# Performance work log

Hardware: AMD Instinct MI355X
Metric: run time of the kernel (lower is better)

Reference implementation:

```python
import jax, jax.numpy as jnp
import numpy as np

B, F, E, V = 16384, 32, 16, 100000
D, S, K = 4, 8, 2            # domains, shared experts, specific experts per domain
I = F * E                    # input_dim = 512
OUT = 16
EPS = 1e-5


def _bn(x):
    # torch BatchNorm1d training mode: biased variance over batch
    m = jnp.mean(x, axis=0)
    v = jnp.var(x, axis=0)
    return (x - m) / jnp.sqrt(v + EPS)


def setup_inputs() -> dict:
    key = jax.random.key(0)
    ks = jax.random.split(key, 24)
    inp = {
        "ids": jax.random.randint(ks[0], (B, F), 0, V),
        "domain_id": jax.random.randint(ks[1], (B,), 0, D),
        "emb_table": jax.random.normal(ks[2], (F, V, E), jnp.float32) * 0.05,
        "domain_weight": jax.random.normal(ks[3], (D, I), jnp.float32) * 0.06,
        "domain_bias": jax.random.uniform(ks[4], (D, I), jnp.float32),
        # shared experts: BN affine + Linear(I->16)
        "sh_gamma": jnp.ones((S, I), jnp.float32),
        "sh_beta": jnp.zeros((S, I), jnp.float32),
        "sh_W": jax.random.normal(ks[5], (S, I, OUT), jnp.float32) * 0.04,
        "sh_b": jnp.zeros((S, OUT), jnp.float32),
        # domain-specific experts
        "sp_gamma": jnp.ones((D, K, I), jnp.float32),
        "sp_beta": jnp.zeros((D, K, I), jnp.float32),
        "sp_W": jax.random.normal(ks[6], (D, K, I, OUT), jnp.float32) * 0.04,
        "sp_b": jnp.zeros((D, K, OUT), jnp.float32),
        # gate
        "gate_W": jax.random.normal(ks[7], (I, S + K), jnp.float32) * 0.04,
        "gate_b": jnp.zeros((S + K,), jnp.float32),
        # final MLP 16 -> 32 -> 32 -> 1 (Linear+BN+ReLU per hidden layer)
        "mlp_W1": jax.random.normal(ks[8], (OUT, 32), jnp.float32) * 0.25,
        "mlp_b1": jnp.zeros((32,), jnp.float32),
        "mlp_g1": jnp.ones((32,), jnp.float32),
        "mlp_be1": jnp.zeros((32,), jnp.float32),
        "mlp_W2": jax.random.normal(ks[9], (32, 32), jnp.float32) * 0.18,
        "mlp_b2": jnp.zeros((32,), jnp.float32),
        "mlp_g2": jnp.ones((32,), jnp.float32),
        "mlp_be2": jnp.zeros((32,), jnp.float32),
        "mlp_W3": jax.random.normal(ks[10], (32, 1), jnp.float32) * 0.18,
        "mlp_b3": jnp.zeros((1,), jnp.float32),
    }
    return inp


def reference(ids, domain_id, emb_table, domain_weight, domain_bias,
              sh_gamma, sh_beta, sh_W, sh_b,
              sp_gamma, sp_beta, sp_W, sp_b,
              gate_W, gate_b,
              mlp_W1, mlp_b1, mlp_g1, mlp_be1,
              mlp_W2, mlp_b2, mlp_g2, mlp_be2,
              mlp_W3, mlp_b3):
    # embedding lookup: per-field table gather -> [B, F, E] -> [B, I]
    emb = emb_table[jnp.arange(F)[None, :], ids].reshape(B, I)

    # torch.where over domain masks collapses to a gather of per-domain affine
    shared_emb = emb * domain_weight[domain_id] + domain_bias[domain_id]  # [B, I]

    # shared experts: BN stats shared (same input), per-expert affine + linear
    xh = _bn(shared_emb)  # [B, I]
    shared_out = (jnp.einsum('bi,si,sio->bso', xh, sh_gamma, sh_W)
                  + (jnp.einsum('si,sio->so', sh_beta, sh_W) + sh_b)[None])  # [B, S, 16]

    # domain-specific experts run on the FULL batch per domain (dense dispatch)
    dom_in = emb[None] * domain_weight[:, None, :] + domain_bias[:, None, :]  # [D, B, I]
    xh_d = jax.vmap(_bn)(dom_in)  # [D, B, I]
    spec = (jnp.einsum('dbi,dki,dkio->dbko', xh_d, sp_gamma, sp_W)
            + (jnp.einsum('dki,dkio->dko', sp_beta, sp_W) + sp_b)[:, None])  # [D, B, K, 16]
    specific_emb = spec[domain_id, jnp.arange(B)]  # [B, K, 16] (masked select)

    expert_out = jnp.concatenate([shared_out, specific_emb], axis=1)  # [B, S+K, 16]
    gate = jax.nn.softmax(shared_emb @ gate_W + gate_b, axis=-1)       # [B, S+K]
    mix = jnp.sum(expert_out * gate[..., None], axis=1)               # [B, 16]

    h = jax.nn.relu(_bn(mix @ mlp_W1 + mlp_b1) * mlp_g1 + mlp_be1)
    h = jax.nn.relu(_bn(h @ mlp_W2 + mlp_b2) * mlp_g2 + mlp_be2)
    logit = (h @ mlp_W3 + mlp_b3)[:, 0]
    return jax.nn.sigmoid(logit)
```

## Files before the change

kernel.cpp:

```cpp
#include <hip/hip_runtime.h>
#include <hip/hip_bf16.h>

#define B_    16384
#define F_    32
#define E_    16
#define V_    100000
#define D_    4
#define S_    8
#define K_    2
#define I_    512
#define OUT_  16
#define SK_   10
#define C_    192
#define OSTR  193
#define EPS_  1e-5f

typedef __attribute__((ext_vector_type(4))) float f32x4;
typedef __attribute__((ext_vector_type(8))) short bf16x8;

__device__ __forceinline__ unsigned short f2bf(float x) {
    unsigned u = __float_as_uint(x);
    unsigned r = (u + 0x7fffu + ((u >> 16) & 1u)) >> 16;
    return (unsigned short)r;
}
__device__ __forceinline__ float bflo(unsigned u) { return __uint_as_float(u << 16); }
__device__ __forceinline__ float bfhi(unsigned u) { return __uint_as_float(u & 0xffff0000u); }

__global__ __launch_bounds__(512) void k_gather(
    const int* __restrict__ ids, const int* __restrict__ dom,
    const float* __restrict__ tbl, unsigned short* __restrict__ emb,
    float* __restrict__ S1G, float* __restrict__ S2G)
{
    const int t = threadIdx.x;
    const int slot = t & 127;
    const int rsub = t >> 7;
    const int f = slot >> 2;
    const int e0 = (slot & 3) << 2;
    float sa[4][4], qa[4][4];
#pragma unroll
    for (int d = 0; d < 4; ++d)
#pragma unroll
        for (int c = 0; c < 4; ++c) { sa[d][c] = 0.f; qa[d][c] = 0.f; }

    const float* fbase = tbl + (size_t)f * V_ * E_ + e0;
    for (int r0 = blockIdx.x * 4; r0 < B_; r0 += 2048) {
        const int r = r0 + rsub;
        const int id = ids[r * F_ + f];
        const float4 v = *(const float4*)(fbase + (size_t)id * E_);
        const int d = dom[r];
        unsigned p0 = (unsigned)f2bf(v.x) | ((unsigned)f2bf(v.y) << 16);
        unsigned p1 = (unsigned)f2bf(v.z) | ((unsigned)f2bf(v.w) << 16);
        *(uint2*)(emb + (size_t)r * I_ + slot * 4) = make_uint2(p0, p1);
#pragma unroll
        for (int dd = 0; dd < 4; ++dd) {
            const float m = (d == dd) ? 1.f : 0.f;
            sa[dd][0] = fmaf(m, v.x, sa[dd][0]); qa[dd][0] = fmaf(m * v.x, v.x, qa[dd][0]);
            sa[dd][1] = fmaf(m, v.y, sa[dd][1]); qa[dd][1] = fmaf(m * v.y, v.y, qa[dd][1]);
            sa[dd][2] = fmaf(m, v.z, sa[dd][2]); qa[dd][2] = fmaf(m * v.z, v.z, qa[dd][2]);
            sa[dd][3] = fmaf(m, v.w, sa[dd][3]); qa[dd][3] = fmaf(m * v.w, v.w, qa[dd][3]);
        }
    }
    __shared__ float red[2][128][36];
    if (rsub >= 2) {
        float* p = red[rsub - 2][slot];
#pragma unroll
        for (int d = 0; d < 4; ++d)
#pragma unroll
            for (int c = 0; c < 4; ++c) { p[d * 4 + c] = sa[d][c]; p[16 + d * 4 + c] = qa[d][c]; }
    }
    __syncthreads();
    if (rsub < 2) {
        float* p = red[rsub][slot];
#pragma unroll
        for (int d = 0; d < 4; ++d)
#pragma unroll
            for (int c = 0; c < 4; ++c) { sa[d][c] += p[d * 4 + c]; qa[d][c] += p[16 + d * 4 + c]; }
    }
    __syncthreads();
    if (rsub == 1) {
        float* p = red[0][slot];
#pragma unroll
        for (int d = 0; d < 4; ++d)
#pragma unroll
            for (int c = 0; c < 4; ++c) { p[d * 4 + c] = sa[d][c]; p[16 + d * 4 + c] = qa[d][c]; }
    }
    __syncthreads();
    if (rsub == 0) {
        float* p = red[0][slot];
        const int g = blockIdx.x & 7;
#pragma unroll
        for (int d = 0; d < 4; ++d)
#pragma unroll
            for (int c = 0; c < 4; ++c) {
                atomicAdd(&S1G[g * 2048 + d * 512 + slot * 4 + c], sa[d][c] + p[d * 4 + c]);
                atomicAdd(&S2G[g * 2048 + d * 512 + slot * 4 + c], qa[d][c] + p[16 + d * 4 + c]);
            }
    }
}

__global__ __launch_bounds__(256) void k_bucket(
    const int* __restrict__ dom, int* __restrict__ cnt, int* __restrict__ rl)
{
    const int r = blockIdx.x * 256 + threadIdx.x;
    const int d = dom[r];
    const int lane = threadIdx.x & 63;
#pragma unroll
    for (int dd = 0; dd < 4; ++dd) {
        unsigned long long mask = __ballot(d == dd);
        if (d == dd) {
            int lead = __ffsll((unsigned long long)mask) - 1;
            int pos = 0;
            if (lane == lead) pos = atomicAdd(&cnt[dd], __popcll(mask));
            pos = __shfl(pos, lead);
            pos += __popcll(mask & ((1ull << lane) - 1ull));
            rl[dd * B_ + pos] = r;
        }
    }
}

__global__ __launch_bounds__(512) void k_stats(
    const float* __restrict__ S1G, const float* __restrict__ S2G, const int* __restrict__ cnt,
    const float* __restrict__ dw, const float* __restrict__ db,
    float* __restrict__ m_, float* __restrict__ dq, float* __restrict__ mu, float* __restrict__ isg)
{
    const int i = threadIdx.x;
    float nd[4], s1v[4], s2v[4], wv[4], bv[4];
#pragma unroll
    for (int d = 0; d < 4; ++d) {
        nd[d] = (float)cnt[d];
        float a = 0.f, b = 0.f;
#pragma unroll
        for (int g = 0; g < 8; ++g) {
            a += S1G[g * 2048 + d * 512 + i];
            b += S2G[g * 2048 + d * 512 + i];
        }
        s1v[d] = a; s2v[d] = b;
        wv[d] = dw[d * I_ + i];  bv[d] = db[d * I_ + i];
    }
    const float invB = 1.0f / (float)B_;
    float tot1 = s1v[0] + s1v[1] + s1v[2] + s1v[3];
    float tot2 = s2v[0] + s2v[1] + s2v[2] + s2v[3];
    float m = tot1 * invB;
    float v = fmaxf(tot2 * invB - m * m, 0.f);
    m_[i] = m;
#pragma unroll
    for (int d = 0; d < 4; ++d)
        dq[d * I_ + i] = wv[d] / sqrtf(v * wv[d] * wv[d] + EPS_);
    float ssum = 0.f, ssq = 0.f;
#pragma unroll
    for (int d = 0; d < 4; ++d) {
        ssum += wv[d] * s1v[d] + nd[d] * bv[d];
        ssq  += wv[d] * wv[d] * s2v[d] + 2.f * wv[d] * bv[d] * s1v[d] + nd[d] * bv[d] * bv[d];
    }
    float muv = ssum * invB;
    float var = fmaxf(ssq * invB - muv * muv, 0.f);
    mu[i] = muv;
    isg[i] = 1.f / sqrtf(var + EPS_);
}

__global__ __launch_bounds__(256) void k_foldM(
    const float* __restrict__ dw, const float* __restrict__ isg, const float* __restrict__ dq,
    const float* __restrict__ shg, const float* __restrict__ shW,
    const float* __restrict__ spg, const float* __restrict__ spW,
    const float* __restrict__ gW, unsigned short* __restrict__ MB)
{
    const int d = blockIdx.y;
    const int ct = blockIdx.x >> 4, ic = blockIdx.x & 15;
    const int t = threadIdx.x;
    const int lane = t >> 2, jp = t & 3;
    const int c = ct * 16 + (lane & 15);
    unsigned short hi2[2], lo2[2];
#pragma unroll
    for (int jj = 0; jj < 2; ++jj) {
        const int i = ic * 32 + (lane >> 4) * 8 + jp * 2 + jj;
        float val = 0.f;
        if (c < 128) {
            const int s = c >> 4, o = c & 15;
            val = dw[d * I_ + i] * isg[i] * shg[s * I_ + i] * shW[((size_t)s * I_ + i) * OUT_ + o];
        } else if (c < 160) {
            const int k = (c - 128) >> 4, o = c & 15;
            val = dq[d * I_ + i] * spg[((size_t)(d * K_ + k)) * I_ + i]
                * spW[(((size_t)(d * K_ + k)) * I_ + i) * OUT_ + o];
        } else if (c < 170) {
            val = dw[d * I_ + i] * gW[i * SK_ + (c - 160)];
        }
        unsigned short h = f2bf(val);
        float hv = __uint_as_float((unsigned)h << 16);
        hi2[jj] = h;
        lo2[jj] = f2bf(val - hv);
    }
    const size_t base = (((size_t)(d * 12 + ct) * 16 + ic) * 2) * 512 + lane * 8 + jp * 2;
    *(ushort2*)(MB + base)       = make_ushort2(hi2[0], hi2[1]);
    *(ushort2*)(MB + base + 512) = make_ushort2(lo2[0], lo2[1]);
}

__global__ __launch_bounds__(256) void k_foldB(
    const float* __restrict__ m_, const float* __restrict__ dq,
    const float* __restrict__ mu, const float* __restrict__ isg,
    const float* __restrict__ db,
    const float* __restrict__ shg, const float* __restrict__ shb_, const float* __restrict__ shW,
    const float* __restrict__ shb2,
    const float* __restrict__ spg, const float* __restrict__ spb_, const float* __restrict__ spW,
    const float* __restrict__ spb2,
    const float* __restrict__ gW, const float* __restrict__ gb, float* __restrict__ bias)
{
    const int d = blockIdx.y, e = blockIdx.x, t = threadIdx.x;
    __shared__ float red[256][17];
    float acc[16];
#pragma unroll
    for (int o = 0; o < 16; ++o) acc[o] = 0.f;

    if (e < 8) {
        for (int i = t; i < I_; i += 256) {
            float coef = (db[d * I_ + i] - mu[i]) * isg[i] * shg[e * I_ + i] + shb_[e * I_ + i];
            const float* wp = &shW[((size_t)e * I_ + i) * OUT_];
#pragma unroll
            for (int o = 0; o < 16; ++o) acc[o] += coef * wp[o];
        }
    } else if (e < 10) {
        const int k = e - 8;
        for (int i = t; i < I_; i += 256) {
            float coef = -m_[i] * dq[d * I_ + i] * spg[((size_t)(d * K_ + k)) * I_ + i]
                       + spb_[((size_t)(d * K_ + k)) * I_ + i];
            const float* wp = &spW[(((size_t)(d * K_ + k)) * I_ + i) * OUT_];
#pragma unroll
            for (int o = 0; o < 16; ++o) acc[o] += coef * wp[o];
        }
    } else {
        for (int i = t; i < I_; i += 256) {
            float bb = db[d * I_ + i];
#pragma unroll
            for (int g = 0; g < 10; ++g) acc[g] += bb * gW[i * SK_ + g];
        }
    }
#pragma unroll
    for (int o = 0; o < 16; ++o) red[t][o] = acc[o];
    __syncthreads();
    for (int st = 128; st > 0; st >>= 1) {
        if (t < st) {
#pragma unroll
            for (int o = 0; o < 16; ++o) red[t][o] += red[t + st][o];
        }
        __syncthreads();
    }
    if (t == 0) {
        if (e < 8) {
            for (int o = 0; o < 16; ++o) bias[d * C_ + e * 16 + o] = red[0][o] + shb2[e * 16 + o];
        } else if (e < 10) {
            const int k = e - 8;
            for (int o = 0; o < 16; ++o)
                bias[d * C_ + 128 + k * 16 + o] = red[0][o] + spb2[(d * K_ + k) * 16 + o];
        } else {
            for (int g = 0; g < 10; ++g) bias[d * C_ + 160 + g] = red[0][g] + gb[g];
            for (int c = 170; c < C_; ++c) bias[d * C_ + c] = 0.f;
        }
    }
}

__global__ __launch_bounds__(512) void k_main(
    const unsigned short* __restrict__ emb, const int* __restrict__ rl, const int* __restrict__ cnt,
    const unsigned short* __restrict__ MB, const float* __restrict__ bias,
    const float* __restrict__ W1, const float* __restrict__ b1,
    float* __restrict__ h1g, float* __restrict__ h1s, float* __restrict__ h1q)
{
    const int d = blockIdx.y, tile = blockIdx.x;
    const int base = tile * 64;
    const int rem = cnt[d] - base;
    if (rem <= 0) return;
    const int nn = rem < 64 ? rem : 64;
    const int t = threadIdx.x;

    __shared__ int rid[64];
    __shared__ float smem[64 * OSTR + 64 * 33];
    float* obuf  = smem;
    float* h1buf = smem + 64 * OSTR;

    if (t < 64) rid[t] = rl[d * B_ + base + (t < nn ? t : nn - 1)];
    __syncthreads();

    const int wv = t >> 6, lane = t & 63;
    const int rt = wv & 3, ch = wv >> 2;
    const int l15 = lane & 15, lk = lane >> 4;

    const unsigned short* arow  = emb + (size_t)rid[rt * 16 + l15] * I_ + lk * 8;
    const unsigned short* bbase = MB + (size_t)d * 196608 + (size_t)ch * 98304 + lane * 8;

    f32x4 acc[6];
#pragma unroll
    for (int c6 = 0; c6 < 6; ++c6) acc[c6] = (f32x4){0.f, 0.f, 0.f, 0.f};

#pragma unroll 2
    for (int ic = 0; ic < 16; ++ic) {
        const bf16x8 a = *(const bf16x8*)(arow + ic * 32);
#pragma unroll
        for (int c6 = 0; c6 < 6; ++c6) {
            const unsigned short* bp = bbase + (size_t)c6 * 16384 + ic * 1024;
            const bf16x8 bh = *(const bf16x8*)bp;
            const bf16x8 bl = *(const bf16x8*)(bp + 512);
            acc[c6] = __builtin_amdgcn_mfma_f32_16x16x32_bf16(a, bh, acc[c6], 0, 0, 0);
            acc[c6] = __builtin_amdgcn_mfma_f32_16x16x32_bf16(a, bl, acc[c6], 0, 0, 0);
        }
    }

    const float* bd = bias + d * C_;
#pragma unroll
    for (int c6 = 0; c6 < 6; ++c6) {
        const int col = ch * 96 + c6 * 16 + l15;
        const float bv = bd[col];
#pragma unroll
        for (int j = 0; j < 4; ++j) {
            const int row = rt * 16 + lk * 4 + j;
            obuf[row * OSTR + col] = acc[c6][j] + bv;
        }
    }
    __syncthreads();

    if (t < 64) {
        const float* row = &obuf[t * OSTR];
        float g[10];
        float mx = row[160];
#pragma unroll
        for (int e = 1; e < 10; ++e) mx = fmaxf(mx, row[160 + e]);
        float ssum = 0.f;
#pragma unroll
        for (int e = 0; e < 10; ++e) { g[e] = __expf(row[160 + e] - mx); ssum += g[e]; }
        const float inv = 1.f / ssum;
        float mix[16];
#pragma unroll
        for (int o = 0; o < 16; ++o) mix[o] = 0.f;
#pragma unroll
        for (int e = 0; e < 10; ++e) {
#pragma unroll
            for (int o = 0; o < 16; ++o) mix[o] = fmaf(g[e], row[e * 16 + o], mix[o]);
        }
#pragma unroll
        for (int o = 0; o < 16; ++o) mix[o] *= inv;
#pragma unroll
        for (int o2 = 0; o2 < 32; ++o2) {
            float a = b1[o2];
#pragma unroll
            for (int o = 0; o < 16; ++o) a = fmaf(mix[o], W1[o * 32 + o2], a);
            h1buf[t * 33 + o2] = a;
        }
    }
    __syncthreads();
    if (t < 32) {
        float s = 0.f, q = 0.f;
        for (int r = 0; r < nn; ++r) { float v = h1buf[r * 33 + t]; s += v; q += v * v; }
        atomicAdd(&h1s[t], s); atomicAdd(&h1q[t], q);
    }
#pragma unroll
    for (int k = 0; k < 4; ++k) {
        const int idx = k * 512 + t;
        const int r = idx >> 5, c = idx & 31;
        if (r < nn) h1g[(size_t)rid[r] * 32 + c] = h1buf[r * 33 + c];
    }
}

__global__ __launch_bounds__(256) void k_mlp1(
    const float* __restrict__ h1g, const float* __restrict__ s1, const float* __restrict__ s2,
    const float* __restrict__ g1, const float* __restrict__ be1,
    const float* __restrict__ W2, const float* __restrict__ b2,
    float* __restrict__ h2g, float* __restrict__ h2s, float* __restrict__ h2q)
{
    __shared__ float hb[64 * 33];
    __shared__ float ab[64 * 33];
    __shared__ float w2t[32 * 32];
    __shared__ float scl[32], shf[32];
    const int t = threadIdx.x;
    const size_t rb = (size_t)blockIdx.x * 64;
#pragma unroll
    for (int k = 0; k < 2; ++k) {
        const int w = k * 1024 + t * 4;
        const int r = w >> 5, c = w & 31;
        *(float4*)&hb[r * 33 + c] = *(const float4*)&h1g[rb * 32 + w];
    }
#pragma unroll
    for (int k = 0; k < 4; ++k) {
        const int idx = k * 256 + t;
        const int i = idx >> 5, o = idx & 31;
        w2t[o * 32 + i] = W2[idx];
    }
    if (t < 32) {
        const float invB = 1.0f / (float)B_;
        float mn = s1[t] * invB;
        float vr = fmaxf(s2[t] * invB - mn * mn, 0.f);
        float iv = 1.f / sqrtf(vr + EPS_);
        scl[t] = iv * g1[t]; shf[t] = be1[t] - mn * iv * g1[t];
    }
    __syncthreads();
    const int r = t >> 2, sub = t & 3;
#pragma unroll
    for (int k = 0; k < 8; ++k) {
        const int i = sub * 8 + k;
        float x = hb[r * 33 + i] * scl[i] + shf[i];
        ab[r * 33 + i] = fmaxf(x, 0.f);
    }
    __syncthreads();
    float h2[8];
#pragma unroll
    for (int kk = 0; kk < 8; ++kk) {
        const int o = sub * 8 + kk;
        float acc = b2[o];
#pragma unroll
        for (int i = 0; i < 32; i += 4) {
            const float4 w4 = *(const float4*)&w2t[o * 32 + i];
            acc = fmaf(ab[r * 33 + i], w4.x, acc);
            acc = fmaf(ab[r * 33 + i + 1], w4.y, acc);
            acc = fmaf(ab[r * 33 + i + 2], w4.z, acc);
            acc = fmaf(ab[r * 33 + i + 3], w4.w, acc);
        }
        h2[kk] = acc;
    }
    __syncthreads();
#pragma unroll
    for (int kk = 0; kk < 8; ++kk) hb[r * 33 + sub * 8 + kk] = h2[kk];
    __syncthreads();
    if (t < 32) {
        float s = 0.f, q = 0.f;
        for (int rr = 0; rr < 64; ++rr) { float v = hb[rr * 33 + t]; s += v; q += v * v; }
        atomicAdd(&h2s[t], s); atomicAdd(&h2q[t], q);
    }
#pragma unroll
    for (int k = 0; k < 2; ++k) {
        const int w = k * 1024 + t * 4;
        const int r2 = w >> 5, c = w & 31;
        *(float4*)&h2g[rb * 32 + w] = *(const float4*)&hb[r2 * 33 + c];
    }
}

__global__ __launch_bounds__(256) void k_mlp2(
    const float* __restrict__ h2g, const float* __restrict__ s1, const float* __restrict__ s2,
    const float* __restrict__ g2, const float* __restrict__ be2,
    const float* __restrict__ W3, const float* __restrict__ b3, float* __restrict__ out)
{
    __shared__ float hb[64 * 33];
    __shared__ float scl[32], shf[32], w3s[32];
    const int t = threadIdx.x;
    const size_t rb = (size_t)blockIdx.x * 64;
#pragma unroll
    for (int k = 0; k < 2; ++k) {
        const int w = k * 1024 + t * 4;
        const int r = w >> 5, c = w & 31;
        *(float4*)&hb[r * 33 + c] = *(const float4*)&h2g[rb * 32 + w];
    }
    if (t < 32) {
        const float invB = 1.0f / (float)B_;
        float mn = s1[t] * invB;
        float vr = fmaxf(s2[t] * invB - mn * mn, 0.f);
        float iv = 1.f / sqrtf(vr + EPS_);
        scl[t] = iv * g2[t]; shf[t] = be2[t] - mn * iv * g2[t];
        w3s[t] = W3[t];
    }
    __syncthreads();
    if (t < 64) {
        float acc = b3[0];
#pragma unroll
        for (int i = 0; i < 32; ++i) {
            float x = hb[t * 33 + i] * scl[i] + shf[i];
            x = fmaxf(x, 0.f);
            acc = fmaf(x, w3s[i], acc);
        }
        out[rb + t] = 1.f / (1.f + __expf(-acc));
    }
}

extern "C" void kernel_launch(void* const* d_in, const int* in_sizes, int n_in,
                              void* d_out, int out_size, void* d_ws, size_t ws_size,
                              hipStream_t stream) {
    const int*   ids  = (const int*)d_in[0];
    const int*   dom  = (const int*)d_in[1];
    const float* tbl  = (const float*)d_in[2];
    const float* dw   = (const float*)d_in[3];
    const float* db   = (const float*)d_in[4];
    const float* shg  = (const float*)d_in[5];
    const float* shb_ = (const float*)d_in[6];
    const float* shW  = (const float*)d_in[7];
    const float* shb2 = (const float*)d_in[8];
    const float* spg  = (const float*)d_in[9];
    const float* spb_ = (const float*)d_in[10];
    const float* spW  = (const float*)d_in[11];
    const float* spb2 = (const float*)d_in[12];
    const float* gW   = (const float*)d_in[13];
    const float* gb   = (const float*)d_in[14];
    const float* W1   = (const float*)d_in[15];
    const float* b1   = (const float*)d_in[16];
    const float* g1   = (const float*)d_in[17];
    const float* be1  = (const float*)d_in[18];
    const float* W2   = (const float*)d_in[19];
    const float* b2   = (const float*)d_in[20];
    const float* g2   = (const float*)d_in[21];
    const float* be2  = (const float*)d_in[22];
    const float* W3   = (const float*)d_in[23];
    const float* b3   = (const float*)d_in[24];
    float* out = (float*)d_out;

    float* ws = (float*)d_ws;
    float* S1G  = ws + 0;
    float* S2G  = ws + 16384;
    float* H1S  = ws + 32768;
    float* H1Q  = ws + 32800;
    float* H2S  = ws + 32832;
    float* H2Q  = ws + 32864;
    int*   CNT  = (int*)(ws + 32896);
    float* M0v  = ws + 32960;
    float* DQ   = ws + 33472;
    float* MU   = ws + 35520;
    float* ISG  = ws + 36032;
    float* BIASW= ws + 36544;
    unsigned short* MB = (unsigned short*)(ws + 37312);
    int*   RL   = (int*)(ws + 430528);
    unsigned short* EMB = (unsigned short*)(ws + 496064);
    float* H1G  = ws + 4690368;
    float* H2G  = ws + 5214656;

    hipMemsetAsync(d_ws, 0, 131600, stream);

    k_gather<<<512, 512, 0, stream>>>(ids, dom, tbl, EMB, S1G, S2G);
    k_bucket<<<64, 256, 0, stream>>>(dom, CNT, RL);
    k_stats<<<1, 512, 0, stream>>>(S1G, S2G, CNT, dw, db, M0v, DQ, MU, ISG);
    k_foldM<<<dim3(192, 4), 256, 0, stream>>>(dw, ISG, DQ, shg, shW, spg, spW, gW, MB);
    k_foldB<<<dim3(11, 4), 256, 0, stream>>>(M0v, DQ, MU, ISG, db, shg, shb_, shW, shb2,
                                             spg, spb_, spW, spb2, gW, gb, BIASW);
    k_main<<<dim3(256, 4), 512, 0, stream>>>(EMB, RL, CNT, MB, BIASW, W1, b1, H1G, H1S, H1Q);
    k_mlp1<<<256, 256, 0, stream>>>(H1G, H1S, H1Q, g1, be1, W2, b2, H2G, H2S, H2Q);
    k_mlp2<<<256, 256, 0, stream>>>(H2G, H2S, H2Q, g2, be2, W3, b3, out);
}
```

Baseline: 403.0 us.

## Batch gather loads, spread atomics, merge fold kernels, halve main tile rows

The gather kernel now issues all eight id and table loads up front so their memory latency overlaps instead of being serialized per loop iteration. Atomic accumulators for the BN statistics are spread over 16 slots instead of 8 or 1, cutting contention. k_bucket does its prefix sums per block in shared memory so it needs one atomic per domain per block. The two fold kernels become one launch, k_stats uses two blocks, and k_main uses 32-row tiles with 3 column groups per wave to double the block count. The costs are higher register pressure in the gather, a larger memset, and repeated B-matrix loads across more tiles in k_main.

Result: faster. 383.0 us (-5.0%).

```diff
diff --git a/kernel.cpp b/kernel.cpp
--- a/kernel.cpp
+++ b/kernel.cpp
@@ -14,6 +14,7 @@
 #define C_    192
 #define OSTR  193
 #define EPS_  1e-5f
+#define NG    16
 
 typedef __attribute__((ext_vector_type(4))) float f32x4;
 typedef __attribute__((ext_vector_type(8))) short bf16x8;
@@ -23,8 +24,6 @@
     unsigned r = (u + 0x7fffu + ((u >> 16) & 1u)) >> 16;
     return (unsigned short)r;
 }
-__device__ __forceinline__ float bflo(unsigned u) { return __uint_as_float(u << 16); }
-__device__ __forceinline__ float bfhi(unsigned u) { return __uint_as_float(u & 0xffff0000u); }
 
 __global__ __launch_bounds__(512) void k_gather(
     const int* __restrict__ ids, const int* __restrict__ dom,
@@ -36,30 +35,45 @@
     const int rsub = t >> 7;
     const int f = slot >> 2;
     const int e0 = (slot & 3) << 2;
+    const int rbase = blockIdx.x * 4 + rsub;
+    const float* fbase = tbl + (size_t)f * V_ * E_ + e0;
+
+    int idv[8];
+#pragma unroll
+    for (int it = 0; it < 8; ++it)
+        idv[it] = ids[(rbase + it * 2048) * F_ + f];
+    float4 v[8];
+#pragma unroll
+    for (int it = 0; it < 8; ++it)
+        v[it] = *(const float4*)(fbase + (size_t)idv[it] * E_);
+    int dv[8];
+#pragma unroll
+    for (int it = 0; it < 8; ++it)
+        dv[it] = dom[rbase + it * 2048];
+
     float sa[4][4], qa[4][4];
 #pragma unroll
     for (int d = 0; d < 4; ++d)
 #pragma unroll
         for (int c = 0; c < 4; ++c) { sa[d][c] = 0.f; qa[d][c] = 0.f; }
 
-    const float* fbase = tbl + (size_t)f * V_ * E_ + e0;
-    for (int r0 = blockIdx.x * 4; r0 < B_; r0 += 2048) {
-        const int r = r0 + rsub;
-        const int id = ids[r * F_ + f];
-        const float4 v = *(const float4*)(fbase + (size_t)id * E_);
-        const int d = dom[r];
-        unsigned p0 = (unsigned)f2bf(v.x) | ((unsigned)f2bf(v.y) << 16);
-        unsigned p1 = (unsigned)f2bf(v.z) | ((unsigned)f2bf(v.w) << 16);
+#pragma unroll
+    for (int it = 0; it < 8; ++it) {
+        const int r = rbase + it * 2048;
+        unsigned p0 = (unsigned)f2bf(v[it].x) | ((unsigned)f2bf(v[it].y) << 16);
+        unsigned p1 = (unsigned)f2bf(v[it].z) | ((unsigned)f2bf(v[it].w) << 16);
         *(uint2*)(emb + (size_t)r * I_ + slot * 4) = make_uint2(p0, p1);
+        const int d = dv[it];
 #pragma unroll
         for (int dd = 0; dd < 4; ++dd) {
             const float m = (d == dd) ? 1.f : 0.f;
-            sa[dd][0] = fmaf(m, v.x, sa[dd][0]); qa[dd][0] = fmaf(m * v.x, v.x, qa[dd][0]);
-            sa[dd][1] = fmaf(m, v.y, sa[dd][1]); qa[dd][1] = fmaf(m * v.y, v.y, qa[dd][1]);
-            sa[dd][2] = fmaf(m, v.z, sa[dd][2]); qa[dd][2] = fmaf(m * v.z, v.z, qa[dd][2]);
-            sa[dd][3] = fmaf(m, v.w, sa[dd][3]); qa[dd][3] = fmaf(m * v.w, v.w, qa[dd][3]);
-        }
-    }
+            sa[dd][0] = fmaf(m, v[it].x, sa[dd][0]); qa[dd][0] = fmaf(m * v[it].x, v[it].x, qa[dd][0]);
+            sa[dd][1] = fmaf(m, v[it].y, sa[dd][1]); qa[dd][1] = fmaf(m * v[it].y, v[it].y, qa[dd][1]);
+            sa[dd][2] = fmaf(m, v[it].z, sa[dd][2]); qa[dd][2] = fmaf(m * v[it].z, v[it].z, qa[dd][2]);
+            sa[dd][3] = fmaf(m, v[it].w, sa[dd][3]); qa[dd][3] = fmaf(m * v[it].w, v[it].w, qa[dd][3]);
+        }
+    }
+
     __shared__ float red[2][128][36];
     if (rsub >= 2) {
         float* p = red[rsub - 2][slot];
@@ -87,13 +101,13 @@
     __syncthreads();
     if (rsub == 0) {
         float* p = red[0][slot];
-        const int g = blockIdx.x & 7;
+        const int g = blockIdx.x & (NG - 1);
 #pragma unroll
         for (int d = 0; d < 4; ++d)
 #pragma unroll
             for (int c = 0; c < 4; ++c) {
-                atomicAdd(&S1G[g * 2048 + d * 512 + slot * 4 + c], sa[d][c] + p[d * 4 + c]);
-                atomicAdd(&S2G[g * 2048 + d * 512 + slot * 4 + c], qa[d][c] + p[16 + d * 4 + c]);
+                atomicAdd(&S1G[(g * 4 + d) * 512 + slot * 4 + c], sa[d][c] + p[d * 4 + c]);
+                atomicAdd(&S2G[(g * 4 + d) * 512 + slot * 4 + c], qa[d][c] + p[16 + d * 4 + c]);
             }
     }
 }
@@ -101,38 +115,44 @@
 __global__ __launch_bounds__(256) void k_bucket(
     const int* __restrict__ dom, int* __restrict__ cnt, int* __restrict__ rl)
 {
-    const int r = blockIdx.x * 256 + threadIdx.x;
+    const int t = threadIdx.x;
+    const int r = blockIdx.x * 256 + t;
     const int d = dom[r];
-    const int lane = threadIdx.x & 63;
+    const int wv = t >> 6;
+    const int lane = t & 63;
+    __shared__ int wcnt[4][4];
+    int myoff = 0;
 #pragma unroll
     for (int dd = 0; dd < 4; ++dd) {
-        unsigned long long mask = __ballot(d == dd);
-        if (d == dd) {
-            int lead = __ffsll((unsigned long long)mask) - 1;
-            int pos = 0;
-            if (lane == lead) pos = atomicAdd(&cnt[dd], __popcll(mask));
-            pos = __shfl(pos, lead);
-            pos += __popcll(mask & ((1ull << lane) - 1ull));
-            rl[dd * B_ + pos] = r;
-        }
-    }
-}
-
-__global__ __launch_bounds__(512) void k_stats(
+        unsigned long long m = __ballot(d == dd);
+        if (lane == 0) wcnt[dd][wv] = (int)__popcll(m);
+        if (d == dd) myoff = (int)__popcll(m & ((1ull << lane) - 1ull));
+    }
+    __syncthreads();
+    if (t < 4) {
+        int c0 = wcnt[t][0], c1 = wcnt[t][1], c2 = wcnt[t][2], c3 = wcnt[t][3];
+        int b = atomicAdd(&cnt[t], c0 + c1 + c2 + c3);
+        wcnt[t][0] = b; wcnt[t][1] = b + c0; wcnt[t][2] = b + c0 + c1; wcnt[t][3] = b + c0 + c1 + c2;
+    }
+    __syncthreads();
+    rl[d * B_ + wcnt[d][wv] + myoff] = r;
+}
+
+__global__ __launch_bounds__(256) void k_stats(
     const float* __restrict__ S1G, const float* __restrict__ S2G, const int* __restrict__ cnt,
     const float* __restrict__ dw, const float* __restrict__ db,
     float* __restrict__ m_, float* __restrict__ dq, float* __restrict__ mu, float* __restrict__ isg)
 {
-    const int i = threadIdx.x;
+    const int i = blockIdx.x * 256 + threadIdx.x;
     float nd[4], s1v[4], s2v[4], wv[4], bv[4];
 #pragma unroll
     for (int d = 0; d < 4; ++d) {
         nd[d] = (float)cnt[d];
         float a = 0.f, b = 0.f;
 #pragma unroll
-        for (int g = 0; g < 8; ++g) {
-            a += S1G[g * 2048 + d * 512 + i];
-            b += S2G[g * 2048 + d * 512 + i];
+        for (int g = 0; g < NG; ++g) {
+            a += S1G[(g * 4 + d) * 512 + i];
+            b += S2G[(g * 4 + d) * 512 + i];
         }
         s1v[d] = a; s2v[d] = b;
         wv[d] = dw[d * I_ + i];  bv[d] = db[d * I_ + i];
@@ -158,53 +178,49 @@
     isg[i] = 1.f / sqrtf(var + EPS_);
 }
 
-__global__ __launch_bounds__(256) void k_foldM(
+__global__ __launch_bounds__(256) void k_fold(
     const float* __restrict__ dw, const float* __restrict__ isg, const float* __restrict__ dq,
     const float* __restrict__ shg, const float* __restrict__ shW,
     const float* __restrict__ spg, const float* __restrict__ spW,
-    const float* __restrict__ gW, unsigned short* __restrict__ MB)
+    const float* __restrict__ gW, unsigned short* __restrict__ MB,
+    const float* __restrict__ m_, const float* __restrict__ mu,
+    const float* __restrict__ db,
+    const float* __restrict__ shb_, const float* __restrict__ shb2,
+    const float* __restrict__ spb_, const float* __restrict__ spb2,
+    const float* __restrict__ gb, float* __restrict__ bias)
 {
     const int d = blockIdx.y;
-    const int ct = blockIdx.x >> 4, ic = blockIdx.x & 15;
     const int t = threadIdx.x;
-    const int lane = t >> 2, jp = t & 3;
-    const int c = ct * 16 + (lane & 15);
-    unsigned short hi2[2], lo2[2];
-#pragma unroll
-    for (int jj = 0; jj < 2; ++jj) {
-        const int i = ic * 32 + (lane >> 4) * 8 + jp * 2 + jj;
-        float val = 0.f;
-        if (c < 128) {
-            const int s = c >> 4, o = c & 15;
-            val = dw[d * I_ + i] * isg[i] * shg[s * I_ + i] * shW[((size_t)s * I_ + i) * OUT_ + o];
-        } else if (c < 160) {
-            const int k = (c - 128) >> 4, o = c & 15;
-            val = dq[d * I_ + i] * spg[((size_t)(d * K_ + k)) * I_ + i]
-                * spW[(((size_t)(d * K_ + k)) * I_ + i) * OUT_ + o];
-        } else if (c < 170) {
-            val = dw[d * I_ + i] * gW[i * SK_ + (c - 160)];
-        }
-        unsigned short h = f2bf(val);
-        float hv = __uint_as_float((unsigned)h << 16);
-        hi2[jj] = h;
-        lo2[jj] = f2bf(val - hv);
-    }
-    const size_t base = (((size_t)(d * 12 + ct) * 16 + ic) * 2) * 512 + lane * 8 + jp * 2;
-    *(ushort2*)(MB + base)       = make_ushort2(hi2[0], hi2[1]);
-    *(ushort2*)(MB + base + 512) = make_ushort2(lo2[0], lo2[1]);
-}
-
-__global__ __launch_bounds__(256) void k_foldB(
-    const float* __restrict__ m_, const float* __restrict__ dq,
-    const float* __restrict__ mu, const float* __restrict__ isg,
-    const float* __restrict__ db,
-    const float* __restrict__ shg, const float* __restrict__ shb_, const float* __restrict__ shW,
-    const float* __restrict__ shb2,
-    const float* __restrict__ spg, const float* __restrict__ spb_, const float* __restrict__ spW,
-    const float* __restrict__ spb2,
-    const float* __restrict__ gW, const float* __restrict__ gb, float* __restrict__ bias)
-{
-    const int d = blockIdx.y, e = blockIdx.x, t = threadIdx.x;
+    if (blockIdx.x < 192) {
+        const int ct = blockIdx.x >> 4, ic = blockIdx.x & 15;
+        const int lane = t >> 2, jp = t & 3;
+        const int c = ct * 16 + (lane & 15);
+        unsigned short hi2[2], lo2[2];
+#pragma unroll
+        for (int jj = 0; jj < 2; ++jj) {
+            const int i = ic * 32 + (lane >> 4) * 8 + jp * 2 + jj;
+            float val = 0.f;
+            if (c < 128) {
+                const int s = c >> 4, o = c & 15;
+                val = dw[d * I_ + i] * isg[i] * shg[s * I_ + i] * shW[((size_t)s * I_ + i) * OUT_ + o];
+            } else if (c < 160) {
+                const int k = (c - 128) >> 4, o = c & 15;
+                val = dq[d * I_ + i] * spg[((size_t)(d * K_ + k)) * I_ + i]
+                    * spW[(((size_t)(d * K_ + k)) * I_ + i) * OUT_ + o];
+            } else if (c < 170) {
+                val = dw[d * I_ + i] * gW[i * SK_ + (c - 160)];
+            }
+            unsigned short h = f2bf(val);
+            float hv = __uint_as_float((unsigned)h << 16);
+            hi2[jj] = h;
+            lo2[jj] = f2bf(val - hv);
+        }
+        const size_t base = (((size_t)(d * 12 + ct) * 16 + ic) * 2) * 512 + lane * 8 + jp * 2;
+        *(ushort2*)(MB + base)       = make_ushort2(hi2[0], hi2[1]);
+        *(ushort2*)(MB + base + 512) = make_ushort2(lo2[0], lo2[1]);
+        return;
+    }
+    const int e = blockIdx.x - 192;
     __shared__ float red[256][17];
     float acc[16];
 #pragma unroll
@@ -264,58 +280,58 @@
     float* __restrict__ h1g, float* __restrict__ h1s, float* __restrict__ h1q)
 {
     const int d = blockIdx.y, tile = blockIdx.x;
-    const int base = tile * 64;
+    const int base = tile * 32;
     const int rem = cnt[d] - base;
     if (rem <= 0) return;
-    const int nn = rem < 64 ? rem : 64;
+    const int nn = rem < 32 ? rem : 32;
     const int t = threadIdx.x;
 
-    __shared__ int rid[64];
-    __shared__ float smem[64 * OSTR + 64 * 33];
+    __shared__ int rid[32];
+    __shared__ float smem[32 * OSTR + 32 * 33];
     float* obuf  = smem;
-    float* h1buf = smem + 64 * OSTR;
-
-    if (t < 64) rid[t] = rl[d * B_ + base + (t < nn ? t : nn - 1)];
+    float* h1buf = smem + 32 * OSTR;
+
+    if (t < 32) rid[t] = rl[d * B_ + base + (t < nn ? t : nn - 1)];
     __syncthreads();
 
     const int wv = t >> 6, lane = t & 63;
-    const int rt = wv & 3, ch = wv >> 2;
+    const int rt = wv & 1, ch = wv >> 1;
     const int l15 = lane & 15, lk = lane >> 4;
 
     const unsigned short* arow  = emb + (size_t)rid[rt * 16 + l15] * I_ + lk * 8;
-    const unsigned short* bbase = MB + (size_t)d * 196608 + (size_t)ch * 98304 + lane * 8;
-
-    f32x4 acc[6];
-#pragma unroll
-    for (int c6 = 0; c6 < 6; ++c6) acc[c6] = (f32x4){0.f, 0.f, 0.f, 0.f};
-
-#pragma unroll 2
+    const unsigned short* bbase = MB + (size_t)d * 196608 + (size_t)(ch * 3) * 16384 + lane * 8;
+
+    f32x4 acc[3];
+#pragma unroll
+    for (int c3 = 0; c3 < 3; ++c3) acc[c3] = (f32x4){0.f, 0.f, 0.f, 0.f};
+
+#pragma unroll 4
     for (int ic = 0; ic < 16; ++ic) {
         const bf16x8 a = *(const bf16x8*)(arow + ic * 32);
 #pragma unroll
-        for (int c6 = 0; c6 < 6; ++c6) {
-            const unsigned short* bp = bbase + (size_t)c6 * 16384 + ic * 1024;
+        for (int c3 = 0; c3 < 3; ++c3) {
+            const unsigned short* bp = bbase + (size_t)c3 * 16384 + ic * 1024;
             const bf16x8 bh = *(const bf16x8*)bp;
             const bf16x8 bl = *(const bf16x8*)(bp + 512);
-            acc[c6] = __builtin_amdgcn_mfma_f32_16x16x32_bf16(a, bh, acc[c6], 0, 0, 0);
-            acc[c6] = __builtin_amdgcn_mfma_f32_16x16x32_bf16(a, bl, acc[c6], 0, 0, 0);
+            acc[c3] = __builtin_amdgcn_mfma_f32_16x16x32_bf16(a, bh, acc[c3], 0, 0, 0);
+            acc[c3] = __builtin_amdgcn_mfma_f32_16x16x32_bf16(a, bl, acc[c3], 0, 0, 0);
         }
     }
 
     const float* bd = bias + d * C_;
 #pragma unroll
-    for (int c6 = 0; c6 < 6; ++c6) {
-        const int col = ch * 96 + c6 * 16 + l15;
+    for (int c3 = 0; c3 < 3; ++c3) {
+        const int col = ch * 48 + c3 * 16 + l15;
         const float bv = bd[col];
 #pragma unroll
         for (int j = 0; j < 4; ++j) {
             const int row = rt * 16 + lk * 4 + j;
-            obuf[row * OSTR + col] = acc[c6][j] + bv;
-        }
-    }
-    __syncthreads();
-
-    if (t < 64) {
+            obuf[row * OSTR + col] = acc[c3][j] + bv;
+        }
+    }
+    __syncthreads();
+
+    if (t < 32) {
         const float* row = &obuf[t * OSTR];
         float g[10];
         float mx = row[160];
@@ -347,10 +363,11 @@
     if (t < 32) {
         float s = 0.f, q = 0.f;
         for (int r = 0; r < nn; ++r) { float v = h1buf[r * 33 + t]; s += v; q += v * v; }
-        atomicAdd(&h1s[t], s); atomicAdd(&h1q[t], q);
-    }
-#pragma unroll
-    for (int k = 0; k < 4; ++k) {
+        const int g = (blockIdx.x + blockIdx.y) & (NG - 1);
+        atomicAdd(&h1s[g * 32 + t], s); atomicAdd(&h1q[g * 32 + t], q);
+    }
+#pragma unroll
+    for (int k = 0; k < 2; ++k) {
         const int idx = k * 512 + t;
         const int r = idx >> 5, c = idx & 31;
         if (r < nn) h1g[(size_t)rid[r] * 32 + c] = h1buf[r * 33 + c];
@@ -382,9 +399,12 @@
         w2t[o * 32 + i] = W2[idx];
     }
     if (t < 32) {
+        float s = 0.f, q = 0.f;
+#pragma unroll
+        for (int g = 0; g < NG; ++g) { s += s1[g * 32 + t]; q += s2[g * 32 + t]; }
         const float invB = 1.0f / (float)B_;
-        float mn = s1[t] * invB;
-        float vr = fmaxf(s2[t] * invB - mn * mn, 0.f);
+        float mn = s * invB;
+        float vr = fmaxf(q * invB - mn * mn, 0.f);
         float iv = 1.f / sqrtf(vr + EPS_);
         scl[t] = iv * g1[t]; shf[t] = be1[t] - mn * iv * g1[t];
     }
@@ -419,7 +439,8 @@
     if (t < 32) {
         float s = 0.f, q = 0.f;
         for (int rr = 0; rr < 64; ++rr) { float v = hb[rr * 33 + t]; s += v; q += v * v; }
-        atomicAdd(&h2s[t], s); atomicAdd(&h2q[t], q);
+        const int g = blockIdx.x & (NG - 1);
+        atomicAdd(&h2s[g * 32 + t], s); atomicAdd(&h2q[g * 32 + t], q);
     }
 #pragma unroll
     for (int k = 0; k < 2; ++k) {
@@ -445,9 +466,12 @@
         *(float4*)&hb[r * 33 + c] = *(const float4*)&h2g[rb * 32 + w];
     }
     if (t < 32) {
+        float s = 0.f, q = 0.f;
+#pragma unroll
+        for (int g = 0; g < NG; ++g) { s += s1[g * 32 + t]; q += s2[g * 32 + t]; }
         const float invB = 1.0f / (float)B_;
-        float mn = s1[t] * invB;
-        float vr = fmaxf(s2[t] * invB - mn * mn, 0.f);
+        float mn = s * invB;
+        float vr = fmaxf(q * invB - mn * mn, 0.f);
         float iv = 1.f / sqrtf(vr + EPS_);
         scl[t] = iv * g2[t]; shf[t] = be2[t] - mn * iv * g2[t];
         w3s[t] = W3[t];
@@ -497,32 +521,31 @@
 
     float* ws = (float*)d_ws;
     float* S1G  = ws + 0;
-    float* S2G  = ws + 16384;
-    float* H1S  = ws + 32768;
-    float* H1Q  = ws + 32800;
-    float* H2S  = ws + 32832;
-    float* H2Q  = ws + 32864;
-    int*   CNT  = (int*)(ws + 32896);
-    float* M0v  = ws + 32960;
-    float* DQ   = ws + 33472;
-    float* MU   = ws + 35520;
-    float* ISG  = ws + 36032;
-    float* BIASW= ws + 36544;
-    unsigned short* MB = (unsigned short*)(ws + 37312);
-    int*   RL   = (int*)(ws + 430528);
-    unsigned short* EMB = (unsigned short*)(ws + 496064);
-    float* H1G  = ws + 4690368;
-    float* H2G  = ws + 5214656;
-
-    hipMemsetAsync(d_ws, 0, 131600, stream);
+    float* S2G  = ws + 32768;
+    float* H1S  = ws + 65536;
+    float* H1Q  = ws + 66048;
+    float* H2S  = ws + 66560;
+    float* H2Q  = ws + 67072;
+    int*   CNT  = (int*)(ws + 67584);
+    float* M0v  = ws + 67600;
+    float* DQ   = ws + 68112;
+    float* MU   = ws + 70160;
+    float* ISG  = ws + 70672;
+    float* BIASW= ws + 71184;
+    unsigned short* MB = (unsigned short*)(ws + 71952);
+    int*   RL   = (int*)(ws + 465168);
+    unsigned short* EMB = (unsigned short*)(ws + 530704);
+    float* H1G  = ws + 4725008;
+    float* H2G  = ws + 5249296;
+
+    hipMemsetAsync(d_ws, 0, 270400, stream);
 
     k_gather<<<512, 512, 0, stream>>>(ids, dom, tbl, EMB, S1G, S2G);
     k_bucket<<<64, 256, 0, stream>>>(dom, CNT, RL);
-    k_stats<<<1, 512, 0, stream>>>(S1G, S2G, CNT, dw, db, M0v, DQ, MU, ISG);
-    k_foldM<<<dim3(192, 4), 256, 0, stream>>>(dw, ISG, DQ, shg, shW, spg, spW, gW, MB);
-    k_foldB<<<dim3(11, 4), 256, 0, stream>>>(M0v, DQ, MU, ISG, db, shg, shb_, shW, shb2,
-                                             spg, spb_, spW, spb2, gW, gb, BIASW);
-    k_main<<<dim3(256, 4), 512, 0, stream>>>(EMB, RL, CNT, MB, BIASW, W1, b1, H1G, H1S, H1Q);
+    k_stats<<<2, 256, 0, stream>>>(S1G, S2G, CNT, dw, db, M0v, DQ, MU, ISG);
+    k_fold<<<dim3(203, 4), 256, 0, stream>>>(dw, ISG, DQ, shg, shW, spg, spW, gW, MB,
+                                             M0v, MU, db, shb_, shb2, spb_, spb2, gb, BIASW);
+    k_main<<<dim3(512, 4), 512, 0, stream>>>(EMB, RL, CNT, MB, BIASW, W1, b1, H1G, H1S, H1Q);
     k_mlp1<<<256, 256, 0, stream>>>(H1G, H1S, H1Q, g1, be1, W2, b2, H2G, H2S, H2Q);
     k_mlp2<<<256, 256, 0, stream>>>(H2G, H2S, H2Q, g2, be2, W3, b3, out);
 }
```
